# Kernel optimization log

Hardware: AMD Instinct MI355X
Metric: run time of the kernel (lower is better)

## Reference

```python
import jax, jax.numpy as jnp
import numpy as np

# SCC (sliding/overlapping channel convolution) config, matching init_kwargs
C_IN = 64
C_OUT = 64
GRP_N = 8
OVERLAP = 4
G = C_IN // GRP_N          # input_grp_unit_dim = channels per sliding window = 8
STEP = G - OVERLAP         # channel stride between consecutive output channels = 4
B, H, W = 32, 128, 128


def setup_inputs() -> dict:
    key = jax.random.key(0)
    k1, k2 = jax.random.split(key)
    x = jax.random.normal(k1, (B, C_IN, H, W), dtype=jnp.float32)
    stdv = 1.0 / np.sqrt(G)  # reset_parameters: uniform(-stdv, stdv)
    weights = jax.random.uniform(k2, (C_OUT, G), dtype=jnp.float32,
                                 minval=-stdv, maxval=stdv)
    return {"x": x, "weights": weights}


def _expand_weights(weights):
    # Scatter the (C_OUT, G) sliding-window weights into a dense (C_OUT, C_IN)
    # channel-mixing matrix. Output channel o reads input channels
    # (o*STEP + j) % C_IN for j in [0, G). This keeps the irregular channel
    # access as a tiny scatter instead of materializing a (B,O,G,H,W) gather.
    o = jnp.arange(C_OUT)[:, None]            # (C_OUT, 1)
    j = jnp.arange(G)[None, :]                # (1, G)
    idx = (o * STEP + j) % C_IN               # (C_OUT, G) wrap-around window
    w_full = jnp.zeros((C_OUT, C_IN), dtype=weights.dtype)
    w_full = w_full.at[jnp.broadcast_to(o, idx.shape), idx].add(weights)
    return w_full


def reference(x, weights):
    w_full = _expand_weights(weights)                 # (C_OUT, C_IN)
    # 1x1 spatial conv == per-pixel channel contraction
    return jnp.einsum('oc,bchw->bohw', w_full, x)     # (B, C_OUT, H, W)
```

## Files before the change

kernel.cpp:

```cpp
#include <hip/hip_runtime.h>
#include <hip/hip_bf16.h>


#define CIN   64
#define COUT  64
#define GW    8
#define HW4   4096

__global__ __launch_bounds__(256) void scc_kernel(
    const float4* __restrict__ x,
    const float*  __restrict__ w,
    float4* __restrict__ out)
{
    __shared__ float ws[COUT * GW];
    for (int i = threadIdx.x; i < COUT * GW; i += blockDim.x)
        ws[i] = w[i];
    __syncthreads();

    const int tid = threadIdx.x;
    const int q0  = tid >> 6;
    const int pi  = blockIdx.x * 64 + (tid & 63);
    const int b   = pi >> 12;
    const int hw4 = pi & (HW4 - 1);

    const float4* xp = x   + ((long)b * CIN) * HW4 + hw4;
    float4*       op = out + ((long)b * COUT) * HW4 + hw4;

    const int cbase = 16 * q0;

    float4 win[8];
#pragma unroll
    for (int k = 0; k < 8; ++k)
        win[k] = xp[(long)((cbase + k) & (CIN - 1)) * HW4];

#pragma unroll
    for (int wi = 0; wi < 4; ++wi) {
        float4 nxt[4];
        if (wi < 3) {
#pragma unroll
            for (int k = 0; k < 4; ++k)
                nxt[k] = xp[(long)((cbase + 4 * wi + 8 + k) & (CIN - 1)) * HW4];
        }

#pragma unroll
        for (int q = 0; q < 4; ++q) {
            int o = 4 * q0 + wi + 16 * q;
            float4 a;
            a.x = 0.f; a.y = 0.f; a.z = 0.f; a.w = 0.f;
#pragma unroll
            for (int j = 0; j < 8; ++j) {
                float wt  = ws[o * GW + j];
                float4 xv = win[(4 * wi + j) & 7];
                a.x = fmaf(wt, xv.x, a.x);
                a.y = fmaf(wt, xv.y, a.y);
                a.z = fmaf(wt, xv.z, a.z);
                a.w = fmaf(wt, xv.w, a.w);
            }
            op[(long)o * HW4] = a;
        }

        if (wi < 3) {
#pragma unroll
            for (int k = 0; k < 4; ++k)
                win[(4 * wi + 8 + k) & 7] = nxt[k];
        }
    }
}

extern "C" void kernel_launch(void* const* d_in, const int* in_sizes, int n_in,
                              void* d_out, int out_size, void* d_ws, size_t ws_size,
                              hipStream_t stream) {
    const float4* x = (const float4*)d_in[0];
    const float*  w = (const float*)d_in[1];
    float4* out     = (float4*)d_out;

    const int block = 256;
    const int grid  = 131072 / 64;

    scc_kernel<<<grid, block, 0, stream>>>(x, w, out);
}
```

Baseline: 51.82 us.

## Process all output channels per thread with float2 pixels and global weights

Each thread now owns a float2 pixel pair and sweeps all 64 output channels with a sliding channel window, so every input channel is loaded once instead of overlapping windows across four waves. Shared-memory weight staging and the barrier are removed; weights are read directly from global memory with uniform indices. The tradeoff is narrower 8-byte vector accesses and a longer per-thread loop with more live registers.

```diff
diff --git a/kernel.cpp b/kernel.cpp
--- a/kernel.cpp
+++ b/kernel.cpp
@@ -5,61 +5,50 @@
 #define CIN   64
 #define COUT  64
 #define GW    8
-#define HW4   4096
+#define HW2   8192
 
 __global__ __launch_bounds__(256) void scc_kernel(
-    const float4* __restrict__ x,
+    const float2* __restrict__ x,
     const float*  __restrict__ w,
-    float4* __restrict__ out)
+    float2* __restrict__ out)
 {
-    __shared__ float ws[COUT * GW];
-    for (int i = threadIdx.x; i < COUT * GW; i += blockDim.x)
-        ws[i] = w[i];
-    __syncthreads();
+    const int t   = blockIdx.x * blockDim.x + threadIdx.x;
+    const int b   = t >> 13;
+    const int hw2 = t & (HW2 - 1);
 
-    const int tid = threadIdx.x;
-    const int q0  = tid >> 6;
-    const int pi  = blockIdx.x * 64 + (tid & 63);
-    const int b   = pi >> 12;
-    const int hw4 = pi & (HW4 - 1);
+    const float2* xp = x   + ((long)b * CIN) * HW2 + hw2;
+    float2*       op = out + ((long)b * COUT) * HW2 + hw2;
 
-    const float4* xp = x   + ((long)b * CIN) * HW4 + hw4;
-    float4*       op = out + ((long)b * COUT) * HW4 + hw4;
-
-    const int cbase = 16 * q0;
-
-    float4 win[8];
+    float2 win[8];
 #pragma unroll
     for (int k = 0; k < 8; ++k)
-        win[k] = xp[(long)((cbase + k) & (CIN - 1)) * HW4];
+        win[k] = xp[(long)k * HW2];
 
 #pragma unroll
-    for (int wi = 0; wi < 4; ++wi) {
-        float4 nxt[4];
-        if (wi < 3) {
+    for (int wi = 0; wi < 16; ++wi) {
+        float2 nxt[4];
+        if (wi < 15) {
 #pragma unroll
             for (int k = 0; k < 4; ++k)
-                nxt[k] = xp[(long)((cbase + 4 * wi + 8 + k) & (CIN - 1)) * HW4];
+                nxt[k] = xp[(long)((4 * wi + 8 + k) & (CIN - 1)) * HW2];
         }
 
 #pragma unroll
         for (int q = 0; q < 4; ++q) {
-            int o = 4 * q0 + wi + 16 * q;
-            float4 a;
-            a.x = 0.f; a.y = 0.f; a.z = 0.f; a.w = 0.f;
+            const int o = wi + 16 * q;
+            float ax = 0.f, ay = 0.f;
 #pragma unroll
             for (int j = 0; j < 8; ++j) {
-                float wt  = ws[o * GW + j];
-                float4 xv = win[(4 * wi + j) & 7];
-                a.x = fmaf(wt, xv.x, a.x);
-                a.y = fmaf(wt, xv.y, a.y);
-                a.z = fmaf(wt, xv.z, a.z);
-                a.w = fmaf(wt, xv.w, a.w);
+                float  wt = w[o * GW + j];
+                float2 xv = win[(4 * wi + j) & 7];
+                ax = fmaf(wt, xv.x, ax);
+                ay = fmaf(wt, xv.y, ay);
             }
-            op[(long)o * HW4] = a;
+            float2 a; a.x = ax; a.y = ay;
+            op[(long)o * HW2] = a;
         }
 
-        if (wi < 3) {
+        if (wi < 15) {
 #pragma unroll
             for (int k = 0; k < 4; ++k)
                 win[(4 * wi + 8 + k) & 7] = nxt[k];
@@ -70,12 +59,13 @@
 extern "C" void kernel_launch(void* const* d_in, const int* in_sizes, int n_in,
                               void* d_out, int out_size, void* d_ws, size_t ws_size,
                               hipStream_t stream) {
-    const float4* x = (const float4*)d_in[0];
+    const float2* x = (const float2*)d_in[0];
     const float*  w = (const float*)d_in[1];
-    float4* out     = (float4*)d_out;
+    float2* out     = (float2*)d_out;
 
+    const int total = 32 * HW2;
     const int block = 256;
-    const int grid  = 131072 / 64;
+    const int grid  = total / block;
 
     scc_kernel<<<grid, block, 0, stream>>>(x, w, out);
 }
```

New measurement: 48.53 us. 6.4% less time.
